# Kernel optimization log

Hardware: AMD Instinct MI355X
Metric: run time of the kernel (lower is better)

## Reference

```python
import jax, jax.numpy as jnp
import numpy as np

EPS = 1e-5
DN = ('NCHW', 'OIHW', 'NCHW')


def _conv(x, w):
    return jax.lax.conv_general_dilated(x, w, (1, 1), 'SAME', dimension_numbers=DN)


def _bn(x, g, b, m, v):
    # eval-mode batchnorm over channel axis 1
    inv = jax.lax.rsqrt(v + EPS)
    return (x - m[:, None, None]) * (g * inv)[:, None, None] + b[:, None, None]


def setup_inputs() -> dict:
    key = jax.random.key(0)
    ks = jax.random.split(key, 32)
    dim, mid, B, H, W = 256, 128, 4, 128, 128
    d = {}
    d['x'] = jax.random.normal(ks[0], (B, dim, H, W), dtype=jnp.float32)

    def bn_params(i, c):
        return (jax.random.uniform(ks[i], (c,), dtype=jnp.float32) + 0.5,
                jax.random.normal(ks[i + 1], (c,), dtype=jnp.float32) * 0.1,
                jax.random.normal(ks[i + 2], (c,), dtype=jnp.float32) * 0.1,
                jax.random.uniform(ks[i + 3], (c,), dtype=jnp.float32) + 0.5)

    d['w_p1'] = jax.random.normal(ks[1], (mid, dim, 3, 3), dtype=jnp.float32) * 0.02
    d['g_p1'], d['b_p1'], d['m_p1'], d['v_p1'] = bn_params(2, mid)
    d['w_p2'] = jax.random.normal(ks[6], (mid, dim, 3, 3), dtype=jnp.float32) * 0.02
    d['g_p2'], d['b_p2'], d['m_p2'], d['v_p2'] = bn_params(7, mid)
    d['w_c1'] = jax.random.normal(ks[11], (dim, mid, 3, 3), dtype=jnp.float32) * 0.02
    d['g_c1'], d['b_c1'], d['m_c1'], d['v_c1'] = bn_params(12, dim)
    d['w_c2'] = jax.random.normal(ks[16], (dim, dim, 1, 1), dtype=jnp.float32) * 0.02
    d['g_c2'], d['b_c2'], d['m_c2'], d['v_c2'] = bn_params(17, dim)
    d['w_p3'] = jax.random.normal(ks[21], (dim, dim, 3, 3), dtype=jnp.float32) * 0.02
    d['g_p3'], d['b_p3'], d['m_p3'], d['v_p3'] = bn_params(22, dim)
    return d


def reference(x,
              w_p1, g_p1, b_p1, m_p1, v_p1,
              w_p2, g_p2, b_p2, m_p2, v_p2,
              w_c1, g_c1, b_c1, m_c1, v_c1,
              w_c2, g_c2, b_c2, m_c2, v_c2,
              w_p3, g_p3, b_p3, m_p3, v_p3):
    # conv-bn-relu branches (dim -> 128)
    p1 = jax.nn.relu(_bn(_conv(x, w_p1), g_p1, b_p1, m_p1, v_p1))
    p2 = jax.nn.relu(_bn(_conv(x, w_p2), g_p2, b_p2, m_p2, v_p2))
    # corner pooling: 'top' = reverse cummax over H (axis 2),
    #                 'left' = reverse cummax over W (axis 3)
    cp1 = jax.lax.cummax(p1, axis=2, reverse=True)
    cp2 = jax.lax.cummax(p2, axis=3, reverse=True)
    bn1 = _bn(_conv(cp1 + cp2, w_c1), g_c1, b_c1, m_c1, v_c1)
    bn2 = _bn(_conv(x, w_c2), g_c2, b_c2, m_c2, v_c2)
    r = jax.nn.relu(bn1 + bn2)
    out = jax.nn.relu(_bn(_conv(r, w_p3), g_p3, b_p3, m_p3, v_p3))
    return out
```

## Files before the change

kernel.cpp:

```cpp
#include <hip/hip_runtime.h>
#include <math.h>

#define HH 128
#define WW 128
#define HWSZ (128*128)

typedef __attribute__((ext_vector_type(8))) short short8;
typedef __attribute__((ext_vector_type(4))) float float4v;
typedef __attribute__((ext_vector_type(2))) unsigned uint2v;

__device__ inline short f2bf(float f) {
  unsigned x = __float_as_uint(f);
  unsigned r = (x + 0x7fffu + ((x >> 16) & 1u)) >> 16;
  return (short)r;
}
__device__ inline float bf2f(unsigned short u) {
  return __uint_as_float(((unsigned)u) << 16);
}
__device__ inline int swz(int row, int g) {
  return row * 32 + ((g ^ ((row >> 1) & 3)) << 3);
}

__global__ __launch_bounds__(256) void prep1_kernel(
    const float* __restrict__ x, short* __restrict__ xbf,
    const float* __restrict__ w_p1, const float* __restrict__ g_p1, const float* __restrict__ v_p1,
    const float* __restrict__ w_p2, const float* __restrict__ g_p2, const float* __restrict__ v_p2,
    short* __restrict__ wb12) {
  const int bid = blockIdx.x;
  const int t = threadIdx.x;
  if (bid < 512) {
    __shared__ short tile[128 * 264];
    const int h = bid & 127, b = bid >> 7;
    #pragma unroll
    for (int it = 0; it < 32; it++) {
      int ci = it * 8 + (t >> 5);
      int w4 = (t & 31) * 4;
      float4v f = *(const float4v*)&x[((size_t)b * 256 + ci) * HWSZ + h * WW + w4];
      tile[(w4 + 0) * 264 + ci] = f2bf(f.x);
      tile[(w4 + 1) * 264 + ci] = f2bf(f.y);
      tile[(w4 + 2) * 264 + ci] = f2bf(f.z);
      tile[(w4 + 3) * 264 + ci] = f2bf(f.w);
    }
    __syncthreads();
    #pragma unroll
    for (int i = 0; i < 16; i++) {
      int idx = t + i * 256;
      int w = idx >> 5, ci8 = (idx & 31) * 8;
      short8 v = *(const short8*)&tile[w * 264 + ci8];
      *(short8*)&xbf[(((size_t)b * HH + h) * WW + w) * 256 + ci8] = v;
    }
  } else {
    int slot = bid - 512;
    const float* w; const float* g; const float* v; int cog;
    int co = slot & 127;
    if (slot < 128) { w = w_p1; g = g_p1; v = v_p1; cog = co; }
    else            { w = w_p2; g = g_p2; v = v_p2; cog = co + 128; }
    float s = g[co] * rsqrtf(v[co] + 1e-5f);
    const float* wr = w + (size_t)co * 2304;
    #pragma unroll
    for (int t9 = 0; t9 < 9; t9++)
      wb12[((size_t)t9 * 256 + cog) * 256 + t] = f2bf(wr[t * 9 + t9] * s);
  }
}

__global__ __launch_bounds__(256) void prep2_kernel(
    const float* __restrict__ w_c1, const float* __restrict__ g_c1, const float* __restrict__ v_c1,
    const float* __restrict__ w_c2, const float* __restrict__ g_c2, const float* __restrict__ v_c2,
    const float* __restrict__ w_p3, const float* __restrict__ g_p3, const float* __restrict__ v_p3,
    short* __restrict__ wbc1, short* __restrict__ wbc2, short* __restrict__ wbp3) {
  const int bid = blockIdx.x;
  const int t = threadIdx.x;
  if (bid < 128) {
    int co = bid * 2 + (t >> 7);
    int ci = t & 127;
    float s = g_c1[co] * rsqrtf(v_c1[co] + 1e-5f);
    const float* wr = w_c1 + (size_t)co * 1152;
    #pragma unroll
    for (int t9 = 0; t9 < 9; t9++)
      wbc1[((size_t)t9 * 256 + co) * 128 + ci] = f2bf(wr[ci * 9 + t9] * s);
  } else if (bid < 192) {
    int base = (bid - 128) * 1024 + t;
    #pragma unroll
    for (int k = 0; k < 4; k++) {
      int e = base + k * 256;
      int co = e >> 8;
      float s = g_c2[co] * rsqrtf(v_c2[co] + 1e-5f);
      wbc2[e] = f2bf(w_c2[e] * s);
    }
  } else {
    int co = bid - 192;
    float s = g_p3[co] * rsqrtf(v_p3[co] + 1e-5f);
    const float* wr = w_p3 + (size_t)co * 2304;
    #pragma unroll
    for (int t9 = 0; t9 < 9; t9++)
      wbp3[((size_t)t9 * 256 + co) * 256 + t] = f2bf(wr[t * 9 + t9] * s);
  }
}

template<int CIN_A, bool PHASE_B, int SHIFT_MODE, bool SPLIT_OUT, bool OUT_F32>
__global__ __launch_bounds__(256, 2) void conv_mfma(
    const short* __restrict__ srcA, const short* __restrict__ xB,
    const short* __restrict__ wbA, const short* __restrict__ wbB,
    const float* __restrict__ g0, const float* __restrict__ b0,
    const float* __restrict__ m0, const float* __restrict__ v0,
    const float* __restrict__ g1, const float* __restrict__ b1,
    const float* __restrict__ m1, const float* __restrict__ v1,
    void* __restrict__ out0, void* __restrict__ out1)
{
  __shared__ short A_s[130 * 32];
  __shared__ short B_s[3 * 256 * 32];

  const int tid  = threadIdx.x;
  const int wave = tid >> 6;
  const int lane = tid & 63;
  const int wm = wave & 1;
  const int wn = wave >> 1;
  const int lr = lane & 15;
  const int lk = lane >> 4;

  const int h  = blockIdx.x & 127;
  const int b  = blockIdx.x >> 7;

  constexpr int ncA = CIN_A / 32;
  const int dystart = (h == 0) ? 1 : 0;
  const int dyend   = (h == HH - 1) ? 2 : 3;
  const int chunksA = (dyend - dystart) * ncA;
  const int total   = chunksA + (PHASE_B ? 8 : 0);

  float4v acc[4][8];
  #pragma unroll
  for (int i = 0; i < 4; i++)
    #pragma unroll
    for (int j = 0; j < 8; j++) acc[i][j] = (float4v)(0.0f);

  short8 rA[3], rB[12];
  const short* aRow = nullptr;
  const short* bBase = nullptr;
  bool curIsA = true;

  auto decode = [&](int t, const short*& ar, const short*& bb, bool& isA) {
    isA = (t < chunksA);
    if (isA) {
      int dy  = dystart + t / ncA;
      int ci0 = (t % ncA) * 32;
      ar = srcA + (((size_t)b * HH + (h + dy - 1)) * WW) * CIN_A + ci0;
      bb = wbA + ((size_t)(dy * 3) * 256) * CIN_A + ci0;
    } else {
      int ci0 = (t - chunksA) * 32;
      ar = xB + (((size_t)b * HH + h) * WW) * 256 + ci0;
      bb = wbB + ci0;
    }
  };

  auto loadRegs = [&](const short* ar, const short* bb, bool isA) {
    if (isA) {
      #pragma unroll
      for (int i = 0; i < 2; i++) {
        int idx = tid + i * 256;
        int w = (idx >> 2) - 1, q = idx & 3;
        rA[i] = ((unsigned)w < (unsigned)WW)
                  ? *(const short8*)(ar + (size_t)w * CIN_A + q * 8) : (short8)(0);
      }
      if (tid < 8) {
        int idx = tid + 512;
        int w = (idx >> 2) - 1, q = idx & 3;
        rA[2] = ((unsigned)w < (unsigned)WW)
                  ? *(const short8*)(ar + (size_t)w * CIN_A + q * 8) : (short8)(0);
      }
      #pragma unroll
      for (int i = 0; i < 12; i++) {
        int idx = tid + i * 256;
        int dx = idx >> 10, rem = idx & 1023;
        int co = rem >> 2, q = rem & 3;
        rB[i] = *(const short8*)(bb + (size_t)(dx * 256 + co) * CIN_A + q * 8);
      }
    } else {
      #pragma unroll
      for (int i = 0; i < 2; i++) {
        int idx = tid + i * 256;
        int wp = idx >> 2, q = idx & 3;
        rA[i] = *(const short8*)(ar + (size_t)wp * 256 + q * 8);
      }
      #pragma unroll
      for (int i = 0; i < 4; i++) {
        int idx = tid + i * 256;
        int co = idx >> 2, q = idx & 3;
        rB[i] = *(const short8*)(bb + (size_t)co * 256 + q * 8);
      }
    }
  };

  auto storeLDS = [&](bool isA) {
    if (isA) {
      #pragma unroll
      for (int i = 0; i < 2; i++) {
        int idx = tid + i * 256;
        *(short8*)&A_s[swz(idx >> 2, idx & 3)] = rA[i];
      }
      if (tid < 8) {
        int idx = tid + 512;
        *(short8*)&A_s[swz(idx >> 2, idx & 3)] = rA[2];
      }
      #pragma unroll
      for (int i = 0; i < 12; i++) {
        int idx = tid + i * 256;
        int dx = idx >> 10, rem = idx & 1023;
        *(short8*)&B_s[swz(dx * 256 + (rem >> 2), rem & 3)] = rB[i];
      }
    } else {
      #pragma unroll
      for (int i = 0; i < 2; i++) {
        int idx = tid + i * 256;
        *(short8*)&A_s[swz(idx >> 2, idx & 3)] = rA[i];
      }
      #pragma unroll
      for (int i = 0; i < 4; i++) {
        int idx = tid + i * 256;
        *(short8*)&B_s[swz(idx >> 2, idx & 3)] = rB[i];
      }
    }
  };

  decode(0, aRow, bBase, curIsA);
  loadRegs(aRow, bBase, curIsA);

  for (int t = 0; t < total; t++) {
    bool isA = curIsA;
    __syncthreads();
    storeLDS(isA);
    __syncthreads();
    if (t + 1 < total) {
      decode(t + 1, aRow, bBase, curIsA);
      loadRegs(aRow, bBase, curIsA);
    }
    const int ndx = isA ? 3 : 1;
    for (int dx = 0; dx < ndx; dx++) {
      short8 af[4];
      #pragma unroll
      for (int mi = 0; mi < 4; mi++)
        af[mi] = *(const short8*)&A_s[swz(wm * 64 + mi * 16 + lr + dx, lk)];
      #pragma unroll
      for (int ni = 0; ni < 8; ni++) {
        short8 bfr = *(const short8*)&B_s[swz(dx * 256 + wn * 128 + ni * 16 + lr, lk)];
        #pragma unroll
        for (int mi = 0; mi < 4; mi++)
          acc[mi][ni] = __builtin_amdgcn_mfma_f32_16x16x32_bf16(af[mi], bfr, acc[mi][ni], 0, 0, 0);
      }
    }
  }

  #pragma unroll
  for (int ni = 0; ni < 8; ni++) {
    int c = wn * 128 + ni * 16 + lr;
    float sh;
    if (SHIFT_MODE == 0) {
      float s = g0[c] * rsqrtf(v0[c] + 1e-5f);
      sh = b0[c] - m0[c] * s;
    } else if (SHIFT_MODE == 1) {
      int cc = c & 127;
      const float* gg = (c < 128) ? g0 : g1;
      const float* bb = (c < 128) ? b0 : b1;
      const float* mm = (c < 128) ? m0 : m1;
      const float* vv = (c < 128) ? v0 : v1;
      float s = gg[cc] * rsqrtf(vv[cc] + 1e-5f);
      sh = bb[cc] - mm[cc] * s;
    } else {
      float s0 = g0[c] * rsqrtf(v0[c] + 1e-5f);
      float s1 = g1[c] * rsqrtf(v1[c] + 1e-5f);
      sh = (b0[c] - m0[c] * s0) + (b1[c] - m1[c] * s1);
    }
    #pragma unroll
    for (int mi = 0; mi < 4; mi++) {
      int px = wm * 64 + mi * 16 + lk * 4;
      float4v v = acc[mi][ni];
      v.x = fmaxf(v.x + sh, 0.0f);
      v.y = fmaxf(v.y + sh, 0.0f);
      v.z = fmaxf(v.z + sh, 0.0f);
      v.w = fmaxf(v.w + sh, 0.0f);
      if (OUT_F32) {
        float* ob = (float*)out0;
        *(float4v*)(ob + ((size_t)b * 256 + c) * HWSZ + (size_t)h * WW + px) = v;
      } else if (SPLIT_OUT) {
        short* ob = (short*)((c < 128) ? out0 : out1);
        size_t base = (((size_t)b * HH + h) * WW + px) * 128 + (c & 127);
        ob[base      ] = f2bf(v.x);
        ob[base + 128 ] = f2bf(v.y);
        ob[base + 256 ] = f2bf(v.z);
        ob[base + 384 ] = f2bf(v.w);
      } else {
        short* ob = (short*)out0;
        size_t base = (((size_t)b * HH + h) * WW + px) * 256 + c;
        ob[base      ] = f2bf(v.x);
        ob[base + 256 ] = f2bf(v.y);
        ob[base + 512 ] = f2bf(v.z);
        ob[base + 768 ] = f2bf(v.w);
      }
    }
  }
}

__global__ __launch_bounds__(256) void colscan_kernel(unsigned* __restrict__ p) {
  __shared__ float sm[8][4][32];
  const int t = threadIdx.x;
  const int seg = t >> 5, cq = t & 31;
  const int w = blockIdx.x;
  const int b = blockIdx.y;
  const uint2v* __restrict__ pv = (const uint2v*)p;
  uint2v* __restrict__ pvw = (uint2v*)p;
  const size_t colbase = ((size_t)b * HH * WW + w) * 32 + cq;
  float m0 = -INFINITY, m1 = -INFINITY, m2 = -INFINITY, m3 = -INFINITY;
  uint2v r[16];
  const int htop = seg * 16 + 15;
  #pragma unroll
  for (int i = 0; i < 16; i++) {
    int h = htop - i;
    uint2v u = pv[colbase + (size_t)h * (WW * 32)];
    m0 = fmaxf(m0, bf2f((unsigned short)(u.x & 0xffff)));
    m1 = fmaxf(m1, bf2f((unsigned short)(u.x >> 16)));
    m2 = fmaxf(m2, bf2f((unsigned short)(u.y & 0xffff)));
    m3 = fmaxf(m3, bf2f((unsigned short)(u.y >> 16)));
    uint2v o;
    o.x = ((unsigned)(unsigned short)f2bf(m1) << 16) | (unsigned short)f2bf(m0);
    o.y = ((unsigned)(unsigned short)f2bf(m3) << 16) | (unsigned short)f2bf(m2);
    r[i] = o;
  }
  sm[seg][0][cq] = m0;
  sm[seg][1][cq] = m1;
  sm[seg][2][cq] = m2;
  sm[seg][3][cq] = m3;
  __syncthreads();
  float s0 = -INFINITY, s1 = -INFINITY, s2 = -INFINITY, s3 = -INFINITY;
  #pragma unroll
  for (int s = 0; s < 7; s++) {
    if (seg + 1 + s < 8) {
      s0 = fmaxf(s0, sm[seg + 1 + s][0][cq]);
      s1 = fmaxf(s1, sm[seg + 1 + s][1][cq]);
      s2 = fmaxf(s2, sm[seg + 1 + s][2][cq]);
      s3 = fmaxf(s3, sm[seg + 1 + s][3][cq]);
    }
  }
  #pragma unroll
  for (int i = 0; i < 16; i++) {
    int h = htop - i;
    float f0 = fmaxf(bf2f((unsigned short)(r[i].x & 0xffff)), s0);
    float f1 = fmaxf(bf2f((unsigned short)(r[i].x >> 16)), s1);
    float f2 = fmaxf(bf2f((unsigned short)(r[i].y & 0xffff)), s2);
    float f3 = fmaxf(bf2f((unsigned short)(r[i].y >> 16)), s3);
    uint2v o;
    o.x = ((unsigned)(unsigned short)f2bf(f1) << 16) | (unsigned short)f2bf(f0);
    o.y = ((unsigned)(unsigned short)f2bf(f3) << 16) | (unsigned short)f2bf(f2);
    pvw[colbase + (size_t)h * (WW * 32)] = o;
  }
}

__global__ __launch_bounds__(256) void rowscan_add_kernel(
    const short* __restrict__ p2, short* __restrict__ p1) {
  __shared__ float pf[128 * 129];
  __shared__ float bm[128];
  const int tid = threadIdx.x;
  const int hb = blockIdx.x;
  const int b  = blockIdx.y;
  const size_t base = (((size_t)b * HH + hb) * WW) * 128;

  #pragma unroll
  for (int i = 0; i < 8; i++) {
    int idx = tid + i * 256;
    int w = idx >> 4, g = idx & 15;
    short8 v = *(const short8*)(p2 + base + (size_t)idx * 8);
    #pragma unroll
    for (int j = 0; j < 8; j++) pf[w * 129 + g * 8 + j] = bf2f((unsigned short)v[j]);
  }
  __syncthreads();
  {
    const int seg = tid >> 7;
    const int c = tid & 127;
    float m = -INFINITY;
    const int wtop = seg * 64 + 63;
    for (int i = 0; i < 64; i++) {
      int a = (wtop - i) * 129 + c;
      m = fmaxf(m, pf[a]);
      pf[a] = m;
    }
    if (seg) bm[c] = m;
  }
  __syncthreads();
  #pragma unroll
  for (int i = 0; i < 8; i++) {
    int idx = tid + i * 256;
    int w = idx >> 4, g = idx & 15;
    short8 ov = *(const short8*)(p1 + base + (size_t)idx * 8);
    short8 rv;
    if (w < 64) {
      #pragma unroll
      for (int j = 0; j < 8; j++) {
        float f = fmaxf(pf[w * 129 + g * 8 + j], bm[g * 8 + j]);
        rv[j] = f2bf(f + bf2f((unsigned short)ov[j]));
      }
    } else {
      #pragma unroll
      for (int j = 0; j < 8; j++)
        rv[j] = f2bf(pf[w * 129 + g * 8 + j] + bf2f((unsigned short)ov[j]));
    }
    *(short8*)(p1 + base + (size_t)idx * 8) = rv;
  }
}

extern "C" void kernel_launch(void* const* d_in, const int* in_sizes, int n_in,
                              void* d_out, int out_size, void* d_ws, size_t ws_size,
                              hipStream_t stream) {
  const float* x    = (const float*)d_in[0];
  const float* w_p1 = (const float*)d_in[1];
  const float* g_p1 = (const float*)d_in[2];
  const float* b_p1 = (const float*)d_in[3];
  const float* m_p1 = (const float*)d_in[4];
  const float* v_p1 = (const float*)d_in[5];
  const float* w_p2 = (const float*)d_in[6];
  const float* g_p2 = (const float*)d_in[7];
  const float* b_p2 = (const float*)d_in[8];
  const float* m_p2 = (const float*)d_in[9];
  const float* v_p2 = (const float*)d_in[10];
  const float* w_c1 = (const float*)d_in[11];
  const float* g_c1 = (const float*)d_in[12];
  const float* b_c1 = (const float*)d_in[13];
  const float* m_c1 = (const float*)d_in[14];
  const float* v_c1 = (const float*)d_in[15];
  const float* w_c2 = (const float*)d_in[16];
  const float* g_c2 = (const float*)d_in[17];
  const float* b_c2 = (const float*)d_in[18];
  const float* m_c2 = (const float*)d_in[19];
  const float* v_c2 = (const float*)d_in[20];
  const float* w_p3 = (const float*)d_in[21];
  const float* g_p3 = (const float*)d_in[22];
  const float* b_p3 = (const float*)d_in[23];
  const float* m_p3 = (const float*)d_in[24];
  const float* v_p3 = (const float*)d_in[25];

  char* ws = (char*)d_ws;
  short* p1  = (short*)(ws + 0);
  short* p2  = (short*)(ws + 16777216);
  short* r   = (short*)(ws + 33554432);
  short* xbf = (short*)(ws + 67108864);
  short* wb12 = r;
  short* wbc1 = p2;
  short* wbc2 = (short*)(ws + 16777216 + 589824);
  short* wbp3 = (short*)(ws + 16777216 + 589824 + 131072);

  prep1_kernel<<<dim3(768), 256, 0, stream>>>(x, xbf,
      w_p1, g_p1, v_p1, w_p2, g_p2, v_p2, wb12);

  conv_mfma<256, false, 1, true, false><<<dim3(512), 256, 0, stream>>>(
      xbf, nullptr, wb12, nullptr,
      g_p1, b_p1, m_p1, v_p1, g_p2, b_p2, m_p2, v_p2, (void*)p1, (void*)p2);

  colscan_kernel<<<dim3(128, 4), 256, 0, stream>>>((unsigned*)p1);
  rowscan_add_kernel<<<dim3(128, 4), 256, 0, stream>>>(p2, p1);

  prep2_kernel<<<dim3(448), 256, 0, stream>>>(
      w_c1, g_c1, v_c1, w_c2, g_c2, v_c2, w_p3, g_p3, v_p3, wbc1, wbc2, wbp3);

  conv_mfma<128, true, 2, false, false><<<dim3(512), 256, 0, stream>>>(
      p1, xbf, wbc1, wbc2,
      g_c1, b_c1, m_c1, v_c1, g_c2, b_c2, m_c2, v_c2, (void*)r, nullptr);

  conv_mfma<256, false, 0, false, true><<<dim3(512), 256, 0, stream>>>(
      r, nullptr, wbp3, nullptr,
      g_p3, b_p3, m_p3, v_p3, nullptr, nullptr, nullptr, nullptr, d_out, nullptr);
}
```

Before: 410.2 us.

## Retile conv kernels to 4 output rows by 128 channels per block

```diff
diff --git a/kernel.cpp b/kernel.cpp
--- a/kernel.cpp
+++ b/kernel.cpp
@@ -98,7 +98,7 @@
 }
 
 template<int CIN_A, bool PHASE_B, int SHIFT_MODE, bool SPLIT_OUT, bool OUT_F32>
-__global__ __launch_bounds__(256, 2) void conv_mfma(
+__global__ __launch_bounds__(512, 2) void conv_mfma(
     const short* __restrict__ srcA, const short* __restrict__ xB,
     const short* __restrict__ wbA, const short* __restrict__ wbB,
     const float* __restrict__ g0, const float* __restrict__ b0,
@@ -107,25 +107,23 @@
     const float* __restrict__ m1, const float* __restrict__ v1,
     void* __restrict__ out0, void* __restrict__ out1)
 {
-  __shared__ short A_s[130 * 32];
-  __shared__ short B_s[3 * 256 * 32];
+  __shared__ short A_s[6 * 4160];
+  __shared__ short B_s[9 * 128 * 32];
 
   const int tid  = threadIdx.x;
   const int wave = tid >> 6;
   const int lane = tid & 63;
-  const int wm = wave & 1;
-  const int wn = wave >> 1;
+  const int orow = wave >> 1;
+  const int ph   = wave & 1;
   const int lr = lane & 15;
   const int lk = lane >> 4;
 
-  const int h  = blockIdx.x & 127;
-  const int b  = blockIdx.x >> 7;
-
-  constexpr int ncA = CIN_A / 32;
-  const int dystart = (h == 0) ? 1 : 0;
-  const int dyend   = (h == HH - 1) ? 2 : 3;
-  const int chunksA = (dyend - dystart) * ncA;
-  const int total   = chunksA + (PHASE_B ? 8 : 0);
+  const int bid = blockIdx.x;
+  const int hg = bid & 31, cg = (bid >> 5) & 1, b = bid >> 6;
+  const int h0 = hg * 4;
+
+  constexpr int chunksA = CIN_A / 32;
+  constexpr int total = chunksA + (PHASE_B ? 8 : 0);
 
   float4v acc[4][8];
   #pragma unroll
@@ -133,115 +131,100 @@
     #pragma unroll
     for (int j = 0; j < 8; j++) acc[i][j] = (float4v)(0.0f);
 
-  short8 rA[3], rB[12];
-  const short* aRow = nullptr;
-  const short* bBase = nullptr;
-  bool curIsA = true;
-
-  auto decode = [&](int t, const short*& ar, const short*& bb, bool& isA) {
-    isA = (t < chunksA);
+  short8 rA[7], rB[9];
+
+  auto loadRegs = [&](int ci0, bool isA) {
     if (isA) {
-      int dy  = dystart + t / ncA;
-      int ci0 = (t % ncA) * 32;
-      ar = srcA + (((size_t)b * HH + (h + dy - 1)) * WW) * CIN_A + ci0;
-      bb = wbA + ((size_t)(dy * 3) * 256) * CIN_A + ci0;
+      #pragma unroll
+      for (int i = 0; i < 6; i++) {
+        int gi = tid + i * 512;
+        int j = gi / 520, rem = gi - j * 520;
+        int w = (rem >> 2) - 1, q = rem & 3;
+        int ir = h0 - 1 + j;
+        bool ok = ((unsigned)ir < 128u) && ((unsigned)w < 128u);
+        rA[i] = ok ? *(const short8*)(srcA + (((size_t)b * HH + ir) * WW + w) * CIN_A + ci0 + q * 8)
+                   : (short8)(0);
+      }
+      if (tid < 48) {
+        int rem = tid + 3072 - 2600;
+        int w = (rem >> 2) - 1, q = rem & 3;
+        int ir = h0 + 4;
+        bool ok = ((unsigned)ir < 128u) && ((unsigned)w < 128u);
+        rA[6] = ok ? *(const short8*)(srcA + (((size_t)b * HH + ir) * WW + w) * CIN_A + ci0 + q * 8)
+                   : (short8)(0);
+      }
+      #pragma unroll
+      for (int i = 0; i < 9; i++)
+        rB[i] = *(const short8*)(wbA + ((size_t)(i * 256 + cg * 128 + (tid >> 2))) * CIN_A + ci0 + (tid & 3) * 8);
     } else {
-      int ci0 = (t - chunksA) * 32;
-      ar = xB + (((size_t)b * HH + h) * WW) * 256 + ci0;
-      bb = wbB + ci0;
-    }
-  };
-
-  auto loadRegs = [&](const short* ar, const short* bb, bool isA) {
-    if (isA) {
-      #pragma unroll
-      for (int i = 0; i < 2; i++) {
-        int idx = tid + i * 256;
-        int w = (idx >> 2) - 1, q = idx & 3;
-        rA[i] = ((unsigned)w < (unsigned)WW)
-                  ? *(const short8*)(ar + (size_t)w * CIN_A + q * 8) : (short8)(0);
-      }
-      if (tid < 8) {
-        int idx = tid + 512;
-        int w = (idx >> 2) - 1, q = idx & 3;
-        rA[2] = ((unsigned)w < (unsigned)WW)
-                  ? *(const short8*)(ar + (size_t)w * CIN_A + q * 8) : (short8)(0);
-      }
-      #pragma unroll
-      for (int i = 0; i < 12; i++) {
-        int idx = tid + i * 256;
-        int dx = idx >> 10, rem = idx & 1023;
-        int co = rem >> 2, q = rem & 3;
-        rB[i] = *(const short8*)(bb + (size_t)(dx * 256 + co) * CIN_A + q * 8);
-      }
-    } else {
-      #pragma unroll
-      for (int i = 0; i < 2; i++) {
-        int idx = tid + i * 256;
-        int wp = idx >> 2, q = idx & 3;
-        rA[i] = *(const short8*)(ar + (size_t)wp * 256 + q * 8);
-      }
-      #pragma unroll
-      for (int i = 0; i < 4; i++) {
-        int idx = tid + i * 256;
-        int co = idx >> 2, q = idx & 3;
-        rB[i] = *(const short8*)(bb + (size_t)co * 256 + q * 8);
-      }
+      #pragma unroll
+      for (int i = 0; i < 4; i++)
+        rA[i] = *(const short8*)(xB + (((size_t)b * HH + h0 + i) * WW + (tid >> 2)) * 256 + ci0 + (tid & 3) * 8);
+      rB[0] = *(const short8*)(wbB + (size_t)(cg * 128 + (tid >> 2)) * 256 + ci0 + (tid & 3) * 8);
     }
   };
 
   auto storeLDS = [&](bool isA) {
     if (isA) {
       #pragma unroll
-      for (int i = 0; i < 2; i++) {
-        int idx = tid + i * 256;
-        *(short8*)&A_s[swz(idx >> 2, idx & 3)] = rA[i];
-      }
-      if (tid < 8) {
-        int idx = tid + 512;
-        *(short8*)&A_s[swz(idx >> 2, idx & 3)] = rA[2];
-      }
-      #pragma unroll
-      for (int i = 0; i < 12; i++) {
-        int idx = tid + i * 256;
-        int dx = idx >> 10, rem = idx & 1023;
-        *(short8*)&B_s[swz(dx * 256 + (rem >> 2), rem & 3)] = rB[i];
-      }
+      for (int i = 0; i < 6; i++) {
+        int gi = tid + i * 512;
+        int j = gi / 520, rem = gi - j * 520;
+        *(short8*)&A_s[j * 4160 + swz(rem >> 2, rem & 3)] = rA[i];
+      }
+      if (tid < 48) {
+        int rem = tid + 3072 - 2600;
+        *(short8*)&A_s[5 * 4160 + swz(rem >> 2, rem & 3)] = rA[6];
+      }
+      #pragma unroll
+      for (int i = 0; i < 9; i++)
+        *(short8*)&B_s[swz(i * 128 + (tid >> 2), tid & 3)] = rB[i];
     } else {
       #pragma unroll
-      for (int i = 0; i < 2; i++) {
-        int idx = tid + i * 256;
-        *(short8*)&A_s[swz(idx >> 2, idx & 3)] = rA[i];
-      }
-      #pragma unroll
-      for (int i = 0; i < 4; i++) {
-        int idx = tid + i * 256;
-        *(short8*)&B_s[swz(idx >> 2, idx & 3)] = rB[i];
-      }
+      for (int i = 0; i < 4; i++)
+        *(short8*)&A_s[(i + 1) * 4160 + swz((tid >> 2) + 1, tid & 3)] = rA[i];
+      *(short8*)&B_s[swz(tid >> 2, tid & 3)] = rB[0];
     }
   };
 
-  decode(0, aRow, bBase, curIsA);
-  loadRegs(aRow, bBase, curIsA);
-
+  loadRegs(0, true);
+
+  #pragma unroll 1
   for (int t = 0; t < total; t++) {
-    bool isA = curIsA;
+    const bool isA = (t < chunksA);
     __syncthreads();
     storeLDS(isA);
     __syncthreads();
     if (t + 1 < total) {
-      decode(t + 1, aRow, bBase, curIsA);
-      loadRegs(aRow, bBase, curIsA);
-    }
-    const int ndx = isA ? 3 : 1;
-    for (int dx = 0; dx < ndx; dx++) {
+      const bool nA = (t + 1 < chunksA);
+      const int ci0 = nA ? (t + 1) * 32 : (t + 1 - chunksA) * 32;
+      loadRegs(ci0, nA);
+    }
+    if (isA) {
+      #pragma unroll
+      for (int dy = 0; dy < 3; dy++)
+        #pragma unroll
+        for (int dx = 0; dx < 3; dx++) {
+          short8 af[4];
+          #pragma unroll
+          for (int mi = 0; mi < 4; mi++)
+            af[mi] = *(const short8*)&A_s[(orow + dy) * 4160 + swz(ph * 64 + mi * 16 + lr + dx, lk)];
+          #pragma unroll
+          for (int ni = 0; ni < 8; ni++) {
+            short8 bfr = *(const short8*)&B_s[swz((dy * 3 + dx) * 128 + ni * 16 + lr, lk)];
+            #pragma unroll
+            for (int mi = 0; mi < 4; mi++)
+              acc[mi][ni] = __builtin_amdgcn_mfma_f32_16x16x32_bf16(af[mi], bfr, acc[mi][ni], 0, 0, 0);
+          }
+        }
+    } else {
       short8 af[4];
       #pragma unroll
       for (int mi = 0; mi < 4; mi++)
-        af[mi] = *(const short8*)&A_s[swz(wm * 64 + mi * 16 + lr + dx, lk)];
+        af[mi] = *(const short8*)&A_s[(orow + 1) * 4160 + swz(ph * 64 + mi * 16 + lr + 1, lk)];
       #pragma unroll
       for (int ni = 0; ni < 8; ni++) {
-        short8 bfr = *(const short8*)&B_s[swz(dx * 256 + wn * 128 + ni * 16 + lr, lk)];
+        short8 bfr = *(const short8*)&B_s[swz(ni * 16 + lr, lk)];
         #pragma unroll
         for (int mi = 0; mi < 4; mi++)
           acc[mi][ni] = __builtin_amdgcn_mfma_f32_16x16x32_bf16(af[mi], bfr, acc[mi][ni], 0, 0, 0);
@@ -249,9 +232,10 @@
     }
   }
 
+  const int h2 = h0 + orow;
   #pragma unroll
   for (int ni = 0; ni < 8; ni++) {
-    int c = wn * 128 + ni * 16 + lr;
+    int c = cg * 128 + ni * 16 + lr;
     float sh;
     if (SHIFT_MODE == 0) {
       float s = g0[c] * rsqrtf(v0[c] + 1e-5f);
@@ -271,7 +255,7 @@
     }
     #pragma unroll
     for (int mi = 0; mi < 4; mi++) {
-      int px = wm * 64 + mi * 16 + lk * 4;
+      int px = ph * 64 + mi * 16 + lk * 4;
       float4v v = acc[mi][ni];
       v.x = fmaxf(v.x + sh, 0.0f);
       v.y = fmaxf(v.y + sh, 0.0f);
@@ -279,17 +263,17 @@
       v.w = fmaxf(v.w + sh, 0.0f);
       if (OUT_F32) {
         float* ob = (float*)out0;
-        *(float4v*)(ob + ((size_t)b * 256 + c) * HWSZ + (size_t)h * WW + px) = v;
+        *(float4v*)(ob + ((size_t)b * 256 + c) * HWSZ + (size_t)h2 * WW + px) = v;
       } else if (SPLIT_OUT) {
         short* ob = (short*)((c < 128) ? out0 : out1);
-        size_t base = (((size_t)b * HH + h) * WW + px) * 128 + (c & 127);
+        size_t base = (((size_t)b * HH + h2) * WW + px) * 128 + (c & 127);
         ob[base      ] = f2bf(v.x);
         ob[base + 128 ] = f2bf(v.y);
         ob[base + 256 ] = f2bf(v.z);
         ob[base + 384 ] = f2bf(v.w);
       } else {
         short* ob = (short*)out0;
-        size_t base = (((size_t)b * HH + h) * WW + px) * 256 + c;
+        size_t base = (((size_t)b * HH + h2) * WW + px) * 256 + c;
         ob[base      ] = f2bf(v.x);
         ob[base + 256 ] = f2bf(v.y);
         ob[base + 512 ] = f2bf(v.z);
@@ -448,7 +432,7 @@
   prep1_kernel<<<dim3(768), 256, 0, stream>>>(x, xbf,
       w_p1, g_p1, v_p1, w_p2, g_p2, v_p2, wb12);
 
-  conv_mfma<256, false, 1, true, false><<<dim3(512), 256, 0, stream>>>(
+  conv_mfma<256, false, 1, true, false><<<dim3(256), 512, 0, stream>>>(
       xbf, nullptr, wb12, nullptr,
       g_p1, b_p1, m_p1, v_p1, g_p2, b_p2, m_p2, v_p2, (void*)p1, (void*)p2);
 
@@ -458,11 +442,11 @@
   prep2_kernel<<<dim3(448), 256, 0, stream>>>(
       w_c1, g_c1, v_c1, w_c2, g_c2, v_c2, w_p3, g_p3, v_p3, wbc1, wbc2, wbp3);
 
-  conv_mfma<128, true, 2, false, false><<<dim3(512), 256, 0, stream>>>(
+  conv_mfma<128, true, 2, false, false><<<dim3(256), 512, 0, stream>>>(
       p1, xbf, wbc1, wbc2,
       g_c1, b_c1, m_c1, v_c1, g_c2, b_c2, m_c2, v_c2, (void*)r, nullptr);
 
-  conv_mfma<256, false, 0, false, true><<<dim3(512), 256, 0, stream>>>(
+  conv_mfma<256, false, 0, false, true><<<dim3(256), 512, 0, stream>>>(
       r, nullptr, wbp3, nullptr,
       g_p3, b_p3, m_p3, v_p3, nullptr, nullptr, nullptr, nullptr, d_out, nullptr);
 }
```

Measured after the change: 524.4 us. 1.28x slower.
